# Performance work log

Measured on AMD Instinct MI355X. Metric: run time of the kernel, lower is better.

Reference implementation:

```python
import jax, jax.numpy as jnp
import numpy as np

K = 3
BN_EPS = 1e-3


def setup_inputs() -> dict:
    key = jax.random.key(0)
    ks = jax.random.split(key, 13)
    B, N1, N2 = 8, 1024, 4096
    C1, C2, Cs = 256, 128, 64
    Ctot = C1 + C2 + Cs  # 448
    H = 256
    return {
        "points1": jax.random.normal(ks[0], (B, 3, N1), jnp.float32),
        "points2": jax.random.normal(ks[1], (B, 3, N2), jnp.float32),
        "features1": jax.random.normal(ks[2], (B, C1, N1), jnp.float32),
        "features2": jax.random.normal(ks[3], (B, C2, N2), jnp.float32),
        "skip_features": jax.random.normal(ks[4], (B, Cs, N2), jnp.float32),
        # 1x1 Conv2d weights are equivalent to dense matrices [out, in]
        "W1": jax.random.normal(ks[5], (H, Ctot), jnp.float32) * 0.05,
        "b1": jax.random.normal(ks[6], (H,), jnp.float32) * 0.05,
        "g1": 1.0 + jax.random.normal(ks[7], (H,), jnp.float32) * 0.05,
        "beta1": jax.random.normal(ks[8], (H,), jnp.float32) * 0.05,
        "W2": jax.random.normal(ks[9], (H, H), jnp.float32) * 0.05,
        "b2": jax.random.normal(ks[10], (H,), jnp.float32) * 0.05,
        "g2": 1.0 + jax.random.normal(ks[11], (H,), jnp.float32) * 0.05,
        "beta2": jax.random.normal(ks[12], (H,), jnp.float32) * 0.05,
    }


def _conv_bn_relu(x, W, b, g, beta):
    # x: [B, N, Cin]; 1x1 conv == dense matmul per point
    y = jnp.einsum("bnc,oc->bno", x, W) + b
    # BatchNorm2d in training mode: batch stats over (batch, spatial) per channel
    mu = jnp.mean(y, axis=(0, 1))
    var = jnp.mean(jnp.square(y - mu), axis=(0, 1))  # biased variance
    y = (y - mu) * jax.lax.rsqrt(var + BN_EPS) * g + beta
    return jax.nn.relu(y)


def reference(points1, points2, features1, features2, skip_features,
              W1, b1, g1, beta1, W2, b2, g2, beta2):
    p1 = jnp.swapaxes(points1, 1, 2)  # [B, N1, 3]
    p2 = jnp.swapaxes(points2, 1, 2)  # [B, N2, 3]
    # pairwise Euclidean distances [B, N2, N1]
    d2 = (jnp.sum(p2 * p2, -1, keepdims=True)
          + jnp.sum(p1 * p1, -1)[:, None, :]
          - 2.0 * jnp.einsum("bnd,bmd->bnm", p2, p1))
    dist = jnp.sqrt(jnp.maximum(d2, 0.0))
    # k smallest distances
    neg_top, ind = jax.lax.top_k(-dist, K)  # ind: [B, N2, K]
    dk = -neg_top
    inv = 1.0 / (dk + 1e-10)
    w = inv / jnp.sum(inv, -1, keepdims=True)  # [B, N2, K]
    f1 = jnp.swapaxes(features1, 1, 2)  # [B, N1, C1]
    gathered = jax.vmap(lambda f, i: f[i])(f1, ind)  # [B, N2, K, C1]
    new = jnp.einsum("bnkc,bnk->bnc", gathered, w)  # inverse-distance interp
    x = jnp.concatenate([new,
                         jnp.swapaxes(features2, 1, 2),
                         jnp.swapaxes(skip_features, 1, 2)], axis=-1)
    x = _conv_bn_relu(x, W1, b1, g1, beta1)
    x = _conv_bn_relu(x, W2, b2, g2, beta2)
    return jnp.swapaxes(x, 1, 2)  # [B, Cout, N2]
```

## Files before the change

### kernel.cpp

```cpp
#include <hip/hip_runtime.h>
#include <cstdint>
#include <cstddef>

#define B_    8
#define N1_   1024
#define N2_   4096
#define C1_   256
#define C2_   128
#define CS_   64
#define CT_   448
#define H_    256
#define ROWS_ (B_ * N2_)

typedef __attribute__((ext_vector_type(8))) short bf16x8;
typedef __attribute__((ext_vector_type(4))) float f32x4;
typedef unsigned short ushort_t;
typedef unsigned int   uint_t;

__device__ __forceinline__ ushort_t f2bf(float f) {
    uint_t u = __float_as_uint(f);
    u = (u + 0x7fffu + ((u >> 16) & 1u)) >> 16;
    return (ushort_t)u;
}
__device__ __forceinline__ float bf2f(ushort_t h) {
    return __uint_as_float(((uint_t)h) << 16);
}

__global__ __launch_bounds__(256) void fused_pre(
    const float* __restrict__ p1, const float* __restrict__ p2,
    int* __restrict__ ind, float* __restrict__ wout,
    const float* __restrict__ f1, const float* __restrict__ f2,
    const float* __restrict__ fs, const float* __restrict__ W1,
    const float* __restrict__ W2, ushort_t* __restrict__ f1t,
    ushort_t* __restrict__ x, ushort_t* __restrict__ W1b, ushort_t* __restrict__ W2b)
{
#pragma clang fp contract(off)
    __shared__ __align__(16) char smem[32000];
    const int t = threadIdx.x;
    const int bid = blockIdx.x;
    if (bid < 1024) {
        float4*   cand  = (float4*)(smem);
        float*    pvals = (float*)(smem + 16512);
        float*    thr   = (float*)(smem + 19584);
        ushort_t* lists = (ushort_t*)(smem + 19712);
        float*    pdd   = (float*)(smem + 25856);
        int*      pdi   = (int*)(smem + 28928);
        const int b  = bid >> 7;
        const int qb = (bid & 127) * 32;
        const float* pb1 = p1 + (size_t)b * 3 * N1_;
        for (int i = t; i < N1_; i += 256) {
            float X = pb1[i], Y = pb1[N1_ + i], Z = pb1[2 * N1_ + i];
            cand[i] = make_float4(X, Y, Z, (X * X + Y * Y) + Z * Z);
        }
        const int q = t & 31, split = t >> 5;
        const int n = qb + q;
        const float* pb2 = p2 + (size_t)b * 3 * N2_;
        const float ax = pb2[n], ay = pb2[N2_ + n], az = pb2[2 * N2_ + n];
        const float s2a = (ax * ax + ay * ay) + az * az;
        const float m2x = -2.0f * ax, m2y = -2.0f * ay, m2z = -2.0f * az;
        __syncthreads();
        const int ibeg = split * 128, iend = ibeg + 128;
        {
            float a0 = 3e38f, a1 = 3e38f, a2 = 3e38f;
            for (int i = ibeg; i < iend; ++i) {
                float4 c = cand[i];
                float fd = fmaf(c.x, m2x, fmaf(c.y, m2y, fmaf(c.z, m2z, s2a + c.w)));
                float o0 = a0, o1 = a1;
                a0 = fminf(o0, fd);
                a1 = __builtin_amdgcn_fmed3f(fd, o0, o1);
                a2 = __builtin_amdgcn_fmed3f(fd, o1, a2);
            }
            pvals[t * 3 + 0] = a0; pvals[t * 3 + 1] = a1; pvals[t * 3 + 2] = a2;
        }
        __syncthreads();
        if (t < 32) {
            float m0 = 3e38f, m1 = 3e38f, m2v = 3e38f;
#pragma unroll
            for (int g = 0; g < 8; ++g)
#pragma unroll
                for (int r = 0; r < 3; ++r) {
                    float v = pvals[(g * 32 + t) * 3 + r];
                    float o0 = m0, o1 = m1;
                    m0 = fminf(o0, v);
                    m1 = __builtin_amdgcn_fmed3f(v, o0, o1);
                    m2v = __builtin_amdgcn_fmed3f(v, o1, m2v);
                }
            thr[t] = m2v + 2e-3f;
        }
        __syncthreads();
        const float th = thr[q];
        ushort_t* mylist = lists + (q * 8 + split) * 12;
        int cnt = 0;
        for (int i = ibeg; i < iend; ++i) {
            float4 c = cand[i];
            float fd = fmaf(c.x, m2x, fmaf(c.y, m2y, fmaf(c.z, m2z, s2a + c.w)));
            if (fd <= th && cnt < 12) { mylist[cnt] = (ushort_t)i; cnt++; }
        }
        float e0 = 3e38f, e1 = 3e38f, e2 = 3e38f;
        int   j0 = 0, j1 = 0, j2 = 0;
        for (int k = 0; k < cnt; ++k) {
            const int i = mylist[k];
            float4 c = cand[i];
            float dot = (ax * c.x + ay * c.y) + az * c.z;
            float dd  = (s2a + c.w) - 2.0f * dot;
            float d   = sqrtf(fmaxf(dd, 0.0f));
            if (d < e0)      { e2 = e1; j2 = j1; e1 = e0; j1 = j0; e0 = d; j0 = i; }
            else if (d < e1) { e2 = e1; j2 = j1; e1 = d;  j1 = i; }
            else if (d < e2) { e2 = d;  j2 = i; }
        }
        pdd[(split * 32 + q) * 3 + 0] = e0; pdi[(split * 32 + q) * 3 + 0] = j0;
        pdd[(split * 32 + q) * 3 + 1] = e1; pdi[(split * 32 + q) * 3 + 1] = j1;
        pdd[(split * 32 + q) * 3 + 2] = e2; pdi[(split * 32 + q) * 3 + 2] = j2;
        __syncthreads();
        if (t < 32) {
            float f0 = 3e38f, f1v = 3e38f, f2v = 3e38f;
            int   k0 = 0, k1 = 0, k2 = 0;
#pragma unroll
            for (int g = 0; g < 8; ++g)
#pragma unroll
                for (int r = 0; r < 3; ++r) {
                    float d = pdd[(g * 32 + t) * 3 + r];
                    int   i = pdi[(g * 32 + t) * 3 + r];
                    if (d < f0)       { f2v = f1v; k2 = k1; f1v = f0; k1 = k0; f0 = d; k0 = i; }
                    else if (d < f1v) { f2v = f1v; k2 = k1; f1v = d;  k1 = i; }
                    else if (d < f2v) { f2v = d;  k2 = i; }
                }
            float inv0 = 1.0f / (f0 + 1e-10f);
            float inv1 = 1.0f / (f1v + 1e-10f);
            float inv2 = 1.0f / (f2v + 1e-10f);
            float s = (inv0 + inv1) + inv2;
            const size_t row = (size_t)b * N2_ + qb + t;
            wout[row * 3 + 0] = inv0 / s;
            wout[row * 3 + 1] = inv1 / s;
            wout[row * 3 + 2] = inv2 / s;
            ind[row * 3 + 0] = k0;
            ind[row * 3 + 1] = k1;
            ind[row * 3 + 2] = k2;
        }
    } else if (bid < 1536) {
        float (*tile)[65] = (float (*)[65])smem;
        const int bid2 = bid - 1024;
        const int b  = bid2 >> 6;
        const int ct = (bid2 >> 4) & 3;
        const int nt = bid2 & 15;
        const int c0 = ct * 64, n0 = nt * 64;
        const float* src = f1 + ((size_t)b * C1_ + c0) * N1_ + n0;
#pragma unroll
        for (int j = 0; j < 16; ++j) {
            int lin = j * 256 + t;
            int ci = lin >> 6, nj = lin & 63;
            tile[ci][nj] = src[(size_t)ci * N1_ + nj];
        }
        __syncthreads();
        ushort_t* dst = f1t + ((size_t)b * N1_ + n0) * C1_ + c0;
#pragma unroll
        for (int j = 0; j < 8; ++j) {
            int lin = j * 256 + t;
            int ni = lin >> 5, cjp = (lin & 31) * 2;
            uint_t u = (uint_t)f2bf(tile[cjp][ni]) | ((uint_t)f2bf(tile[cjp + 1][ni]) << 16);
            *(uint_t*)&dst[(size_t)ni * C1_ + cjp] = u;
        }
    } else if (bid < 3072) {
        float (*tile)[65] = (float (*)[65])smem;
        const int bid2 = bid - 1536;
        const int b   = bid2 / 192;
        const int rem = bid2 - b * 192;
        const int ct  = rem >> 6;
        const int nt  = rem & 63;
        const float* src;
        int coff;
        if (ct < 2) { src = f2 + ((size_t)b * C2_ + ct * 64) * N2_; coff = C1_ + ct * 64; }
        else        { src = fs + (size_t)b * CS_ * N2_;             coff = C1_ + C2_; }
        const int n0 = nt * 64;
#pragma unroll
        for (int j = 0; j < 16; ++j) {
            int lin = j * 256 + t;
            int ci = lin >> 6, nj = lin & 63;
            tile[ci][nj] = src[(size_t)ci * N2_ + n0 + nj];
        }
        __syncthreads();
#pragma unroll
        for (int j = 0; j < 8; ++j) {
            int lin = j * 256 + t;
            int ni = lin >> 5, cjp = (lin & 31) * 2;
            uint_t u = (uint_t)f2bf(tile[cjp][ni]) | ((uint_t)f2bf(tile[cjp + 1][ni]) << 16);
            *(uint_t*)&x[((size_t)b * N2_ + n0 + ni) * CT_ + coff + cjp] = u;
        }
    } else {
        const int i = (bid - 3072) * 256 + t;
        if (i < H_ * CT_) W1b[i] = f2bf(W1[i]);
        if (i < H_ * H_)  W2b[i] = f2bf(W2[i]);
    }
}

__global__ __launch_bounds__(256) void gather_x(
    const ushort_t* __restrict__ f1t, const int* __restrict__ ind,
    const float* __restrict__ w, ushort_t* __restrict__ x)
{
    const int t = threadIdx.x;
    const int row = blockIdx.x * 8 + (t >> 5);
    const int b = row >> 12;
    const int cg = (t & 31) * 8;
    const int*   ip = ind + (size_t)row * 3;
    const float* wp = w   + (size_t)row * 3;
    const int i0 = ip[0], i1 = ip[1], i2 = ip[2];
    const float w0 = wp[0], w1 = wp[1], w2 = wp[2];
    const ushort_t* base = f1t + (size_t)b * N1_ * C1_;
    uint4 va = *(const uint4*)(base + (size_t)i0 * C1_ + cg);
    uint4 vb = *(const uint4*)(base + (size_t)i1 * C1_ + cg);
    uint4 vc = *(const uint4*)(base + (size_t)i2 * C1_ + cg);
    const uint_t* pa = (const uint_t*)&va;
    const uint_t* pb = (const uint_t*)&vb;
    const uint_t* pc = (const uint_t*)&vc;
    uint_t out[4];
#pragma unroll
    for (int e = 0; e < 4; ++e) {
        float lo = w0 * bf2f((ushort_t)(pa[e] & 0xffff))
                 + w1 * bf2f((ushort_t)(pb[e] & 0xffff))
                 + w2 * bf2f((ushort_t)(pc[e] & 0xffff));
        float hi = w0 * bf2f((ushort_t)(pa[e] >> 16))
                 + w1 * bf2f((ushort_t)(pb[e] >> 16))
                 + w2 * bf2f((ushort_t)(pc[e] >> 16));
        out[e] = (uint_t)f2bf(lo) | ((uint_t)f2bf(hi) << 16);
    }
    *(uint4*)&x[(size_t)row * CT_ + cg] = *(uint4*)out;
}

__global__ __launch_bounds__(256, 4) void gemm_bf16(
    const ushort_t* __restrict__ A, const ushort_t* __restrict__ Bw,
    const float* __restrict__ bias, ushort_t* __restrict__ C,
    float* __restrict__ ssum, float* __restrict__ ssq, int K)
{
    __shared__ __align__(16) ushort_t smem[128 * 72];
    ushort_t* As = smem;
    ushort_t* Bs = smem + 5120;
    ushort_t* Cs = smem;
    const int t = threadIdx.x;
    const int m0 = (blockIdx.x >> 2) * 128;
    const int n0 = (blockIdx.x & 3) * 64;
    const int lane = t & 63;
    const int wv = t >> 6;
    const int wrow = wv & 1, wcol = wv >> 1;
    const int lm = lane & 15, lq = lane >> 4;
    const int crow = t >> 2, ckc = (t & 3) * 8;
    f32x4 acc[4][2];
#pragma unroll
    for (int i = 0; i < 4; ++i)
#pragma unroll
        for (int j = 0; j < 2; ++j)
            acc[i][j] = (f32x4){0.f, 0.f, 0.f, 0.f};

    for (int k0 = 0; k0 < K; k0 += 32) {
        uint4 a0 = *(const uint4*)(A  + (size_t)(m0 + crow) * K + k0 + ckc);
        uint4 a1 = *(const uint4*)(A  + (size_t)(m0 + 64 + crow) * K + k0 + ckc);
        uint4 b0 = *(const uint4*)(Bw + (size_t)(n0 + crow) * K + k0 + ckc);
        __syncthreads();
        *(uint4*)&As[crow * 40 + ckc]        = a0;
        *(uint4*)&As[(64 + crow) * 40 + ckc] = a1;
        *(uint4*)&Bs[crow * 40 + ckc]        = b0;
        __syncthreads();
        bf16x8 af[4], bfr[2];
#pragma unroll
        for (int i = 0; i < 4; ++i)
            af[i] = *(const bf16x8*)&As[(wrow * 64 + i * 16 + lm) * 40 + lq * 8];
#pragma unroll
        for (int j = 0; j < 2; ++j)
            bfr[j] = *(const bf16x8*)&Bs[(wcol * 32 + j * 16 + lm) * 40 + lq * 8];
#pragma unroll
        for (int i = 0; i < 4; ++i)
#pragma unroll
            for (int j = 0; j < 2; ++j)
                acc[i][j] = __builtin_amdgcn_mfma_f32_16x16x32_bf16(af[i], bfr[j], acc[i][j], 0, 0, 0);
    }
    __syncthreads();
#pragma unroll
    for (int j = 0; j < 2; ++j) {
        const int gn_l = wcol * 32 + j * 16 + lm;
        const int gn   = n0 + gn_l;
        const float bb = bias[gn];
        float ps = 0.0f, pq = 0.0f;
#pragma unroll
        for (int i = 0; i < 4; ++i) {
            const int row_l = wrow * 64 + i * 16 + lq * 4;
            f32x4 v = acc[i][j];
#pragma unroll
            for (int r = 0; r < 4; ++r) {
                float val = v[r] + bb;
                ps += val;
                pq += val * val;
                float vo = __shfl_xor(val, 1);
                uint_t packed = (lm & 1)
                    ? ((uint_t)f2bf(vo)  | ((uint_t)f2bf(val) << 16))
                    : ((uint_t)f2bf(val) | ((uint_t)f2bf(vo)  << 16));
                if ((lm & 1) == 0)
                    *(uint_t*)&Cs[(row_l + r) * 72 + (gn_l & ~1)] = packed;
            }
        }
        ps += __shfl_xor(ps, 16); pq += __shfl_xor(pq, 16);
        ps += __shfl_xor(ps, 32); pq += __shfl_xor(pq, 32);
        if (lane < 16) {
            atomicAdd(&ssum[gn], ps);
            atomicAdd(&ssq[gn], pq);
        }
    }
    __syncthreads();
    const int srow = t >> 3;
    const int scol = (t & 7) * 8;
#pragma unroll
    for (int rep = 0; rep < 4; ++rep) {
        const int row = srow + rep * 32;
        uint4 v = *(const uint4*)&Cs[row * 72 + scol];
        *(uint4*)(C + (size_t)(m0 + row) * H_ + n0 + scol) = v;
    }
}

__global__ __launch_bounds__(256) void bn_relu_mid(
    const ushort_t* __restrict__ y, const float* __restrict__ ssum,
    const float* __restrict__ ssq, const float* __restrict__ g,
    const float* __restrict__ beta, ushort_t* __restrict__ yn)
{
    __shared__ float sc[H_], sh[H_];
    const int t = threadIdx.x;
    {
        const float invN = 1.0f / (float)ROWS_;
        float mu  = ssum[t] * invN;
        float var = ssq[t] * invN - mu * mu;
        float s   = rsqrtf(var + 1e-3f) * g[t];
        sc[t] = s;
        sh[t] = beta[t] - mu * s;
    }
    __syncthreads();
    const int c0 = (t & 31) * 8;
    float s[8], h[8];
#pragma unroll
    for (int e = 0; e < 8; ++e) { s[e] = sc[c0 + e]; h[e] = sh[c0 + e]; }
    const uint4* yin = (const uint4*)y;
    uint4* yout = (uint4*)yn;
    const size_t base = (size_t)blockIdx.x * 2048 + t;
#pragma unroll
    for (int j = 0; j < 8; ++j) {
        uint4 u = yin[base + j * 256];
        uint_t* uw = (uint_t*)&u;
        uint_t o[4];
#pragma unroll
        for (int e = 0; e < 4; ++e) {
            float lo = __uint_as_float(uw[e] << 16);
            float hi = __uint_as_float(uw[e] & 0xffff0000u);
            float rlo = fmaxf(fmaf(lo, s[2 * e],     h[2 * e]),     0.0f);
            float rhi = fmaxf(fmaf(hi, s[2 * e + 1], h[2 * e + 1]), 0.0f);
            o[e] = (uint_t)f2bf(rlo) | ((uint_t)f2bf(rhi) << 16);
        }
        yout[base + j * 256] = *(uint4*)o;
    }
}

__global__ __launch_bounds__(256) void bn_out_kernel(
    const ushort_t* __restrict__ y, const float* __restrict__ ssum, const float* __restrict__ ssq,
    const float* __restrict__ g, const float* __restrict__ beta, float* __restrict__ out)
{
    __shared__ float tile[64][65];
    __shared__ float sc[64], sh[64];
    const float invN = 1.0f / (float)ROWS_;
    const int bid = blockIdx.x;
    const int b  = bid >> 8;
    const int nt = (bid >> 2) & 63;
    const int ot = bid & 3;
    const int t = threadIdx.x;
    if (t < 64) {
        int c = ot * 64 + t;
        float mu  = ssum[c] * invN;
        float var = ssq[c] * invN - mu * mu;
        float s   = rsqrtf(var + 1e-3f) * g[c];
        sc[t] = s;
        sh[t] = beta[c] - mu * s;
    }
    __syncthreads();
    const int n0 = nt * 64, o0 = ot * 64;
    const ushort_t* yb = y + ((size_t)b * N2_ + n0) * H_ + o0;
#pragma unroll
    for (int j = 0; j < 8; ++j) {
        int lin = j * 256 + t;
        int nl = lin >> 5, cu = (lin & 31) * 2;
        uint_t u = *(const uint_t*)&yb[(size_t)nl * H_ + cu];
        tile[nl][cu]     = fmaxf(bf2f((ushort_t)(u & 0xffff)) * sc[cu]     + sh[cu],     0.0f);
        tile[nl][cu + 1] = fmaxf(bf2f((ushort_t)(u >> 16))    * sc[cu + 1] + sh[cu + 1], 0.0f);
    }
    __syncthreads();
    float* ob = out + ((size_t)b * H_ + o0) * N2_ + n0;
#pragma unroll
    for (int j = 0; j < 16; ++j) {
        int lin = j * 256 + t;
        int ol = lin >> 6, nl = lin & 63;
        ob[(size_t)ol * N2_ + nl] = tile[nl][ol];
    }
}

extern "C" void kernel_launch(void* const* d_in, const int* in_sizes, int n_in,
                              void* d_out, int out_size, void* d_ws, size_t ws_size,
                              hipStream_t stream)
{
    (void)in_sizes; (void)n_in; (void)out_size; (void)ws_size;
    const float* points1   = (const float*)d_in[0];
    const float* points2   = (const float*)d_in[1];
    const float* features1 = (const float*)d_in[2];
    const float* features2 = (const float*)d_in[3];
    const float* skipf     = (const float*)d_in[4];
    const float* W1  = (const float*)d_in[5];
    const float* b1  = (const float*)d_in[6];
    const float* g1  = (const float*)d_in[7];
    const float* be1 = (const float*)d_in[8];
    const float* W2  = (const float*)d_in[9];
    const float* b2  = (const float*)d_in[10];
    const float* g2  = (const float*)d_in[11];
    const float* be2 = (const float*)d_in[12];
    float* out = (float*)d_out;

    char* ws = (char*)d_ws;
    float*    s1  = (float*)(ws + 0);
    float*    q1  = (float*)(ws + 1024);
    float*    s2  = (float*)(ws + 2048);
    float*    q2  = (float*)(ws + 3072);
    int*      ind = (int*)(ws + 4096);
    float*    wgt = (float*)(ws + 397312);
    ushort_t* x   = (ushort_t*)(ws + 790528);
    ushort_t* y1b = (ushort_t*)(ws + 30150656);
    ushort_t* y1n = (ushort_t*)(ws + 46927872);
    ushort_t* W1b = (ushort_t*)(ws + 63705088);
    ushort_t* W2b = (ushort_t*)(ws + 63934464);
    ushort_t* f1t = (ushort_t*)(ws + 64065536);
    ushort_t* y2b = x;

    hipMemsetAsync(ws, 0, 4096, stream);

    fused_pre<<<dim3(3520), dim3(256), 0, stream>>>(points1, points2, ind, wgt,
                                                    features1, features2, skipf,
                                                    W1, W2, f1t, x, W1b, W2b);
    gather_x<<<dim3(4096), dim3(256), 0, stream>>>(f1t, ind, wgt, x);

    gemm_bf16<<<dim3(ROWS_ / 128 * 4), dim3(256), 0, stream>>>(x, W1b, b1, y1b, s1, q1, CT_);
    bn_relu_mid<<<dim3(512), dim3(256), 0, stream>>>(y1b, s1, q1, g1, be1, y1n);
    gemm_bf16<<<dim3(ROWS_ / 128 * 4), dim3(256), 0, stream>>>(y1n, W2b, b2, y2b, s2, q2, H_);
    bn_out_kernel<<<dim3(2048), dim3(256), 0, stream>>>(y2b, s2, q2, g2, be2, out);
}
```

Baseline: 208.6 us.

## Fuse BN1+ReLU into second GEMM A-load and use direct-to-LDS loads

Removes the separate bn_relu_mid pass by applying the first layer's BN scale/shift and ReLU while staging the A tile inside the second GEMM, which avoids one full write and re-read of the intermediate activation. Both GEMMs now load operand tiles with global_load_lds into an XOR-swizzled unpadded LDS layout instead of going through registers. The catch is that gemm2 recomputes the BN transform once per N-block (four times per row tile), and the swizzled addressing adds indexing complexity.

```diff
diff --git a/kernel.cpp b/kernel.cpp
--- a/kernel.cpp
+++ b/kernel.cpp
@@ -24,6 +24,11 @@
 }
 __device__ __forceinline__ float bf2f(ushort_t h) {
     return __uint_as_float(((uint_t)h) << 16);
+}
+__device__ __forceinline__ void glds16(const void* g, void* l) {
+    __builtin_amdgcn_global_load_lds(
+        (const __attribute__((address_space(1))) void*)g,
+        (__attribute__((address_space(3))) void*)l, 16, 0, 0);
 }
 
 __global__ __launch_bounds__(256) void fused_pre(
@@ -226,14 +231,14 @@
     *(uint4*)&x[(size_t)row * CT_ + cg] = *(uint4*)out;
 }
 
-__global__ __launch_bounds__(256, 4) void gemm_bf16(
+__global__ __launch_bounds__(256, 4) void gemm1_glds(
     const ushort_t* __restrict__ A, const ushort_t* __restrict__ Bw,
     const float* __restrict__ bias, ushort_t* __restrict__ C,
-    float* __restrict__ ssum, float* __restrict__ ssq, int K)
+    float* __restrict__ ssum, float* __restrict__ ssq)
 {
     __shared__ __align__(16) ushort_t smem[128 * 72];
     ushort_t* As = smem;
-    ushort_t* Bs = smem + 5120;
+    ushort_t* Bs = smem + 4096;
     ushort_t* Cs = smem;
     const int t = threadIdx.x;
     const int m0 = (blockIdx.x >> 2) * 128;
@@ -242,7 +247,15 @@
     const int wv = t >> 6;
     const int wrow = wv & 1, wcol = wv >> 1;
     const int lm = lane & 15, lq = lane >> 4;
-    const int crow = t >> 2, ckc = (t & 3) * 8;
+    const int lrow  = lane >> 2;
+    const int gchunk = (lane & 3) ^ ((lane >> 3) & 3);
+    const int csw = (lm >> 1) & 3;
+    const ushort_t* gA0 = A  + (size_t)(m0 + wv * 16 + lrow) * CT_ + gchunk * 8;
+    const ushort_t* gA1 = A  + (size_t)(m0 + 64 + wv * 16 + lrow) * CT_ + gchunk * 8;
+    const ushort_t* gB  = Bw + (size_t)(n0 + wv * 16 + lrow) * CT_ + gchunk * 8;
+    ushort_t* lA0 = As + wv * 512;
+    ushort_t* lA1 = As + 2048 + wv * 512;
+    ushort_t* lB  = Bs + wv * 512;
     f32x4 acc[4][2];
 #pragma unroll
     for (int i = 0; i < 4; ++i)
@@ -250,22 +263,19 @@
         for (int j = 0; j < 2; ++j)
             acc[i][j] = (f32x4){0.f, 0.f, 0.f, 0.f};
 
-    for (int k0 = 0; k0 < K; k0 += 32) {
-        uint4 a0 = *(const uint4*)(A  + (size_t)(m0 + crow) * K + k0 + ckc);
-        uint4 a1 = *(const uint4*)(A  + (size_t)(m0 + 64 + crow) * K + k0 + ckc);
-        uint4 b0 = *(const uint4*)(Bw + (size_t)(n0 + crow) * K + k0 + ckc);
-        __syncthreads();
-        *(uint4*)&As[crow * 40 + ckc]        = a0;
-        *(uint4*)&As[(64 + crow) * 40 + ckc] = a1;
-        *(uint4*)&Bs[crow * 40 + ckc]        = b0;
+    for (int k0 = 0; k0 < CT_; k0 += 32) {
+        __syncthreads();
+        glds16(gA0 + k0, lA0);
+        glds16(gA1 + k0, lA1);
+        glds16(gB  + k0, lB);
         __syncthreads();
         bf16x8 af[4], bfr[2];
 #pragma unroll
         for (int i = 0; i < 4; ++i)
-            af[i] = *(const bf16x8*)&As[(wrow * 64 + i * 16 + lm) * 40 + lq * 8];
+            af[i] = *(const bf16x8*)&As[(wrow * 64 + i * 16 + lm) * 32 + (lq ^ csw) * 8];
 #pragma unroll
         for (int j = 0; j < 2; ++j)
-            bfr[j] = *(const bf16x8*)&Bs[(wcol * 32 + j * 16 + lm) * 40 + lq * 8];
+            bfr[j] = *(const bf16x8*)&Bs[(wcol * 32 + j * 16 + lm) * 32 + (lq ^ csw) * 8];
 #pragma unroll
         for (int i = 0; i < 4; ++i)
 #pragma unroll
@@ -314,43 +324,128 @@
     }
 }
 
-__global__ __launch_bounds__(256) void bn_relu_mid(
-    const ushort_t* __restrict__ y, const float* __restrict__ ssum,
-    const float* __restrict__ ssq, const float* __restrict__ g,
-    const float* __restrict__ beta, ushort_t* __restrict__ yn)
+__global__ __launch_bounds__(256, 4) void gemm2_fused(
+    const ushort_t* __restrict__ A, const ushort_t* __restrict__ Bw,
+    const float* __restrict__ bias,
+    const float* __restrict__ s1, const float* __restrict__ q1,
+    const float* __restrict__ g1, const float* __restrict__ be1,
+    ushort_t* __restrict__ C, float* __restrict__ ssum, float* __restrict__ ssq)
 {
-    __shared__ float sc[H_], sh[H_];
+    __shared__ __align__(16) ushort_t smem[128 * 72];
+    ushort_t* As = smem;
+    ushort_t* Bs = smem + 5120;
+    float*    sc = (float*)(smem + 7168);
+    float*    sh = (float*)(smem + 7680);
+    ushort_t* Cs = smem;
     const int t = threadIdx.x;
+    const int m0 = (blockIdx.x >> 2) * 128;
+    const int n0 = (blockIdx.x & 3) * 64;
+    const int lane = t & 63;
+    const int wv = t >> 6;
+    const int wrow = wv & 1, wcol = wv >> 1;
+    const int lm = lane & 15, lq = lane >> 4;
+    const int lrow  = lane >> 2;
+    const int gchunk = (lane & 3) ^ ((lane >> 3) & 3);
+    const int csw = (lm >> 1) & 3;
+    const int arow = t >> 1, ahalf = (t & 1) * 16;
     {
         const float invN = 1.0f / (float)ROWS_;
-        float mu  = ssum[t] * invN;
-        float var = ssq[t] * invN - mu * mu;
-        float s   = rsqrtf(var + 1e-3f) * g[t];
+        float mu  = s1[t] * invN;
+        float var = q1[t] * invN - mu * mu;
+        float s   = rsqrtf(var + 1e-3f) * g1[t];
         sc[t] = s;
-        sh[t] = beta[t] - mu * s;
+        sh[t] = be1[t] - mu * s;
+    }
+    const ushort_t* gB = Bw + (size_t)(n0 + wv * 16 + lrow) * H_ + gchunk * 8;
+    ushort_t* lB = Bs + wv * 512;
+    const ushort_t* gA = A + (size_t)(m0 + arow) * H_ + ahalf;
+    f32x4 acc[4][2];
+#pragma unroll
+    for (int i = 0; i < 4; ++i)
+#pragma unroll
+        for (int j = 0; j < 2; ++j)
+            acc[i][j] = (f32x4){0.f, 0.f, 0.f, 0.f};
+
+    for (int k0 = 0; k0 < H_; k0 += 32) {
+        uint4 a0 = *(const uint4*)(gA + k0);
+        uint4 a1 = *(const uint4*)(gA + k0 + 8);
+        __syncthreads();
+        glds16(gB + k0, lB);
+        {
+            const uint_t* w0 = (const uint_t*)&a0;
+            const uint_t* w1 = (const uint_t*)&a1;
+            uint_t o0[4], o1[4];
+#pragma unroll
+            for (int e = 0; e < 4; ++e) {
+                const int cb0 = k0 + ahalf + 2 * e;
+                const int cb1 = cb0 + 8;
+                float lo0 = __uint_as_float(w0[e] << 16);
+                float hi0 = __uint_as_float(w0[e] & 0xffff0000u);
+                float lo1 = __uint_as_float(w1[e] << 16);
+                float hi1 = __uint_as_float(w1[e] & 0xffff0000u);
+                float r0 = fmaxf(fmaf(lo0, sc[cb0],     sh[cb0]),     0.0f);
+                float r1 = fmaxf(fmaf(hi0, sc[cb0 + 1], sh[cb0 + 1]), 0.0f);
+                float r2 = fmaxf(fmaf(lo1, sc[cb1],     sh[cb1]),     0.0f);
+                float r3 = fmaxf(fmaf(hi1, sc[cb1 + 1], sh[cb1 + 1]), 0.0f);
+                o0[e] = (uint_t)f2bf(r0) | ((uint_t)f2bf(r1) << 16);
+                o1[e] = (uint_t)f2bf(r2) | ((uint_t)f2bf(r3) << 16);
+            }
+            *(uint4*)&As[arow * 40 + ahalf]     = *(uint4*)o0;
+            *(uint4*)&As[arow * 40 + ahalf + 8] = *(uint4*)o1;
+        }
+        __syncthreads();
+        bf16x8 af[4], bfr[2];
+#pragma unroll
+        for (int i = 0; i < 4; ++i)
+            af[i] = *(const bf16x8*)&As[(wrow * 64 + i * 16 + lm) * 40 + lq * 8];
+#pragma unroll
+        for (int j = 0; j < 2; ++j)
+            bfr[j] = *(const bf16x8*)&Bs[(wcol * 32 + j * 16 + lm) * 32 + (lq ^ csw) * 8];
+#pragma unroll
+        for (int i = 0; i < 4; ++i)
+#pragma unroll
+            for (int j = 0; j < 2; ++j)
+                acc[i][j] = __builtin_amdgcn_mfma_f32_16x16x32_bf16(af[i], bfr[j], acc[i][j], 0, 0, 0);
     }
     __syncthreads();
-    const int c0 = (t & 31) * 8;
-    float s[8], h[8];
-#pragma unroll
-    for (int e = 0; e < 8; ++e) { s[e] = sc[c0 + e]; h[e] = sh[c0 + e]; }
-    const uint4* yin = (const uint4*)y;
-    uint4* yout = (uint4*)yn;
-    const size_t base = (size_t)blockIdx.x * 2048 + t;
-#pragma unroll
-    for (int j = 0; j < 8; ++j) {
-        uint4 u = yin[base + j * 256];
-        uint_t* uw = (uint_t*)&u;
-        uint_t o[4];
-#pragma unroll
-        for (int e = 0; e < 4; ++e) {
-            float lo = __uint_as_float(uw[e] << 16);
-            float hi = __uint_as_float(uw[e] & 0xffff0000u);
-            float rlo = fmaxf(fmaf(lo, s[2 * e],     h[2 * e]),     0.0f);
-            float rhi = fmaxf(fmaf(hi, s[2 * e + 1], h[2 * e + 1]), 0.0f);
-            o[e] = (uint_t)f2bf(rlo) | ((uint_t)f2bf(rhi) << 16);
-        }
-        yout[base + j * 256] = *(uint4*)o;
+#pragma unroll
+    for (int j = 0; j < 2; ++j) {
+        const int gn_l = wcol * 32 + j * 16 + lm;
+        const int gn   = n0 + gn_l;
+        const float bb = bias[gn];
+        float ps = 0.0f, pq = 0.0f;
+#pragma unroll
+        for (int i = 0; i < 4; ++i) {
+            const int row_l = wrow * 64 + i * 16 + lq * 4;
+            f32x4 v = acc[i][j];
+#pragma unroll
+            for (int r = 0; r < 4; ++r) {
+                float val = v[r] + bb;
+                ps += val;
+                pq += val * val;
+                float vo = __shfl_xor(val, 1);
+                uint_t packed = (lm & 1)
+                    ? ((uint_t)f2bf(vo)  | ((uint_t)f2bf(val) << 16))
+                    : ((uint_t)f2bf(val) | ((uint_t)f2bf(vo)  << 16));
+                if ((lm & 1) == 0)
+                    *(uint_t*)&Cs[(row_l + r) * 72 + (gn_l & ~1)] = packed;
+            }
+        }
+        ps += __shfl_xor(ps, 16); pq += __shfl_xor(pq, 16);
+        ps += __shfl_xor(ps, 32); pq += __shfl_xor(pq, 32);
+        if (lane < 16) {
+            atomicAdd(&ssum[gn], ps);
+            atomicAdd(&ssq[gn], pq);
+        }
+    }
+    __syncthreads();
+    const int srow = t >> 3;
+    const int scol = (t & 7) * 8;
+#pragma unroll
+    for (int rep = 0; rep < 4; ++rep) {
+        const int row = srow + rep * 32;
+        uint4 v = *(const uint4*)&Cs[row * 72 + scol];
+        *(uint4*)(C + (size_t)(m0 + row) * H_ + n0 + scol) = v;
     }
 }
 
@@ -424,7 +519,6 @@
     float*    wgt = (float*)(ws + 397312);
     ushort_t* x   = (ushort_t*)(ws + 790528);
     ushort_t* y1b = (ushort_t*)(ws + 30150656);
-    ushort_t* y1n = (ushort_t*)(ws + 46927872);
     ushort_t* W1b = (ushort_t*)(ws + 63705088);
     ushort_t* W2b = (ushort_t*)(ws + 63934464);
     ushort_t* f1t = (ushort_t*)(ws + 64065536);
@@ -437,8 +531,7 @@
                                                     W1, W2, f1t, x, W1b, W2b);
     gather_x<<<dim3(4096), dim3(256), 0, stream>>>(f1t, ind, wgt, x);
 
-    gemm_bf16<<<dim3(ROWS_ / 128 * 4), dim3(256), 0, stream>>>(x, W1b, b1, y1b, s1, q1, CT_);
-    bn_relu_mid<<<dim3(512), dim3(256), 0, stream>>>(y1b, s1, q1, g1, be1, y1n);
-    gemm_bf16<<<dim3(ROWS_ / 128 * 4), dim3(256), 0, stream>>>(y1n, W2b, b2, y2b, s2, q2, H_);
+    gemm1_glds<<<dim3(ROWS_ / 128 * 4), dim3(256), 0, stream>>>(x, W1b, b1, y1b, s1, q1);
+    gemm2_fused<<<dim3(ROWS_ / 128 * 4), dim3(256), 0, stream>>>(y1b, W2b, b2, s1, q1, g1, be1, y2b, s2, q2);
     bn_out_kernel<<<dim3(2048), dim3(256), 0, stream>>>(y2b, s2, q2, g2, be2, out);
 }
```

Result: no change. 205.0 us (-1.7%).
